# Kernel tuning notes

Hardware: AMD Instinct MI355X
Metric: run time of the kernel (lower is better)

The kernel has to match this reference:

```python
import jax, jax.numpy as jnp
import numpy as np

B, KEY, D, U, MODES = 16384, 64, 128, 128, 32

def setup_inputs() -> dict:
    key = jax.random.key(0)
    k1, k2, k3, k4, k5 = jax.random.split(key, 5)
    return {
        "key": jax.random.normal(k1, (B, KEY), dtype=jnp.float32),
        "x": jax.random.normal(k2, (B, D), dtype=jnp.float32),
        "sens": jnp.ones((MODES,), dtype=jnp.float32),
        "keys_map": jax.random.normal(k3, (MODES, KEY), dtype=jnp.float32),
        "kernels": jax.random.normal(k4, (MODES, D, U), dtype=jnp.float32) * 0.05,
        "biases": jax.random.normal(k5, (MODES, U), dtype=jnp.float32) * 0.05,
    }

def reference(key, x, sens, keys_map, kernels, biases):
    # key: [B, KEY]; keys_map: [MODES, KEY]
    # Euclidean distance of each key to each mode's stored key.
    dist = jnp.sqrt(jnp.sum((key[:, None, :] - keys_map[None, :, :]) ** 2, axis=-1))  # [B, MODES]
    sim = jax.nn.softmax(sens / (dist + 1.0), axis=-1)  # [B, MODES]
    modes = kernels.shape[0]
    # Original: kernel_b = mean_m(sim[b,m] * kernels[m]); out_b = x_b @ kernel_b.
    # Reordered as GEMM-per-mode + weighted combine (same math):
    out = jnp.einsum('bm,bd,mdu->bu', sim, x, kernels) / modes  # [B, U]
    out = out + (sim @ biases) / modes  # mean over modes of sim-weighted biases
    return out
```

## Files before the change

### kernel.cpp

```cpp
#include <hip/hip_runtime.h>

#define BATCH 16384
#define KEYD  64
#define DDIM  128
#define UDIM  128
#define MODES 32

typedef __attribute__((ext_vector_type(8))) short bf16x8;
typedef __attribute__((ext_vector_type(4))) float f32x4;

__device__ __forceinline__ unsigned short f2bf(float f) {
  unsigned u = __float_as_uint(f);
  unsigned r = (u + 0x7FFFu + ((u >> 16) & 1u)) >> 16;
  return (unsigned short)r;
}

__device__ __forceinline__ void gld_lds16(const void* g, void* l) {
  __builtin_amdgcn_global_load_lds(
      (const __attribute__((address_space(1))) unsigned int*)g,
      (__attribute__((address_space(3))) unsigned int*)l, 16, 0, 0);
}

__global__ __launch_bounds__(256) void prep_sim_x(
    const float* __restrict__ key, const float* __restrict__ x,
    const float* __restrict__ sens, const float* __restrict__ keys_map,
    float* __restrict__ sim, unsigned short* __restrict__ x16) {
  __shared__ float kmT[KEYD * MODES];
  int t = threadIdx.x;
  for (int i = t; i < MODES * KEYD; i += 256) {
    int m = i >> 6, k = i & 63;
    kmT[k * MODES + m] = keys_map[i];
  }
  __syncthreads();

  int lane = t & 63;
  int wave = t >> 6;
  int half = lane >> 5;
  int m = lane & 31;
  int row = blockIdx.x * 8 + wave * 2 + half;

  const float* krow = key + (long)row * KEYD;
  float d2 = 0.f;
  #pragma unroll
  for (int k = 0; k < KEYD; ++k) {
    float diff = krow[k] - kmT[k * MODES + m];
    d2 += diff * diff;
  }
  float logit = sens[m] / (sqrtf(d2) + 1.0f);
  float mx = logit;
  #pragma unroll
  for (int off = 16; off > 0; off >>= 1) mx = fmaxf(mx, __shfl_xor(mx, off, 64));
  float e = __expf(logit - mx);
  float s = e;
  #pragma unroll
  for (int off = 16; off > 0; off >>= 1) s += __shfl_xor(s, off, 64);
  sim[(long)row * MODES + m] = e / s;

  const float4 xv = *(const float4*)(x + (long)row * DDIM + m * 4);
  ushort4 o;
  o.x = f2bf(xv.x); o.y = f2bf(xv.y); o.z = f2bf(xv.z); o.w = f2bf(xv.w);
  *(ushort4*)(x16 + (long)row * DDIM + m * 4) = o;
}

__global__ __launch_bounds__(256) void prep_wb(
    const float* __restrict__ kernels, const float* __restrict__ biases,
    unsigned short* __restrict__ kb16, unsigned short* __restrict__ bb16) {
  int t = blockIdx.x * 256 + threadIdx.x;
  if (t < MODES * 16 * UDIM) {
    int u = t & 127, kb = (t >> 7) & 15, m = t >> 11;
    const float* src = kernels + (long)((m * 16 + kb) * 8) * UDIM + u;
    ushort4 lo, hi;
    lo.x = f2bf(src[0 * UDIM]); lo.y = f2bf(src[1 * UDIM]);
    lo.z = f2bf(src[2 * UDIM]); lo.w = f2bf(src[3 * UDIM]);
    hi.x = f2bf(src[4 * UDIM]); hi.y = f2bf(src[5 * UDIM]);
    hi.z = f2bf(src[6 * UDIM]); hi.w = f2bf(src[7 * UDIM]);
    *(ushort4*)(kb16 + (long)t * 8) = lo;
    *(ushort4*)(kb16 + (long)t * 8 + 4) = hi;
  } else if (t < MODES * 16 * UDIM + 4 * UDIM) {
    int tb = t - MODES * 16 * UDIM;
    int u = tb & 127, kb = tb >> 7;
    const float* src = biases + kb * 8 * UDIM + u;
    ushort4 lo, hi;
    lo.x = f2bf(src[0 * UDIM]); lo.y = f2bf(src[1 * UDIM]);
    lo.z = f2bf(src[2 * UDIM]); lo.w = f2bf(src[3 * UDIM]);
    hi.x = f2bf(src[4 * UDIM]); hi.y = f2bf(src[5 * UDIM]);
    hi.z = f2bf(src[6 * UDIM]); hi.w = f2bf(src[7 * UDIM]);
    *(ushort4*)(bb16 + (long)tb * 8) = lo;
    *(ushort4*)(bb16 + (long)tb * 8 + 4) = hi;
  }
}

__global__ __launch_bounds__(256, 2) void gemm_poly(
    const unsigned short* __restrict__ x16, const unsigned short* __restrict__ kb16,
    const unsigned short* __restrict__ bb16, const float* __restrict__ sim,
    float* __restrict__ out) {
  __shared__ alignas(16) unsigned short bsh[16 * UDIM * 8];
  __shared__ alignas(16) float simT[8][128];

  const int t = threadIdx.x;
  const int lane = t & 63, w = t >> 6;
  const int q = lane >> 4, l16 = lane & 15;
  const int wrow = (w >> 1) * 64, wcol = (w & 1) * 64;
  const long bm = (long)blockIdx.x * 128;
  const int split = blockIdx.y;

  {
    int rrow = t >> 1, mg = (t & 1) * 4;
    const float4 v = *(const float4*)(sim + (bm + rrow) * MODES + split * 8 + mg);
    simT[mg + 0][rrow] = v.x; simT[mg + 1][rrow] = v.y;
    simT[mg + 2][rrow] = v.z; simT[mg + 3][rrow] = v.w;
  }

  bf16x8 aF[4][4];
  #pragma unroll
  for (int rt = 0; rt < 4; ++rt)
    #pragma unroll
    for (int ks = 0; ks < 4; ++ks)
      aF[rt][ks] = *(const bf16x8*)(x16 + (bm + wrow + rt * 16 + l16) * DDIM + ks * 32 + q * 8);

  f32x4 acc[4][4] = {};

  for (int mi = 0; mi < 8; ++mi) {
    const int m = split * 8 + mi;
    __syncthreads();
    const unsigned short* src = kb16 + (long)m * (16 * UDIM * 8);
    #pragma unroll
    for (int i = 0; i < 8; ++i) {
      int off = (t + i * 256) * 8;
      gld_lds16(src + off, bsh + off);
    }
    __syncthreads();

    bf16x8 bF[4][4];
    #pragma unroll
    for (int ks = 0; ks < 4; ++ks)
      #pragma unroll
      for (int ct = 0; ct < 4; ++ct)
        bF[ks][ct] = *(const bf16x8*)&bsh[(((ks * 4 + q) * UDIM) + wcol + ct * 16 + l16) * 8];

    #pragma unroll
    for (int rt = 0; rt < 4; ++rt) {
      f32x4 tmp[4] = {};
      #pragma unroll
      for (int ks = 0; ks < 4; ++ks)
        #pragma unroll
        for (int ct = 0; ct < 4; ++ct)
          tmp[ct] = __builtin_amdgcn_mfma_f32_16x16x32_bf16(aF[rt][ks], bF[ks][ct], tmp[ct], 0, 0, 0);
      const f32x4 s = *(const f32x4*)&simT[mi][wrow + rt * 16 + q * 4];
      #pragma unroll
      for (int ct = 0; ct < 4; ++ct)
        acc[rt][ct] += s * tmp[ct];
    }
  }

  if (split == 0) {
    bf16x8 sF[4];
    #pragma unroll
    for (int rt = 0; rt < 4; ++rt) {
      const float* sp = sim + (bm + wrow + rt * 16 + l16) * MODES + q * 8;
      bf16x8 f;
      #pragma unroll
      for (int j = 0; j < 8; ++j) f[j] = (short)f2bf(sp[j]);
      sF[rt] = f;
    }
    #pragma unroll
    for (int ct = 0; ct < 4; ++ct) {
      bf16x8 bb = *(const bf16x8*)(bb16 + (long)(q * UDIM + wcol + ct * 16 + l16) * 8);
      #pragma unroll
      for (int rt = 0; rt < 4; ++rt)
        acc[rt][ct] = __builtin_amdgcn_mfma_f32_16x16x32_bf16(sF[rt], bb, acc[rt][ct], 0, 0, 0);
    }
  }

  #pragma unroll
  for (int rt = 0; rt < 4; ++rt)
    #pragma unroll
    for (int ct = 0; ct < 4; ++ct) {
      long row = bm + wrow + rt * 16 + q * 4;
      int col = wcol + ct * 16 + l16;
      #pragma unroll
      for (int r = 0; r < 4; ++r)
        atomicAdd(out + (row + r) * UDIM + col, acc[rt][ct][r] * (1.0f / MODES));
    }
}

extern "C" void kernel_launch(void* const* d_in, const int* in_sizes, int n_in,
                              void* d_out, int out_size, void* d_ws, size_t ws_size,
                              hipStream_t stream) {
  const float* key      = (const float*)d_in[0];
  const float* x        = (const float*)d_in[1];
  const float* sens     = (const float*)d_in[2];
  const float* keys_map = (const float*)d_in[3];
  const float* kernels  = (const float*)d_in[4];
  const float* biases   = (const float*)d_in[5];
  float* out = (float*)d_out;

  char* ws = (char*)d_ws;
  float*          sim  = (float*)ws;
  unsigned short* x16  = (unsigned short*)(ws + (2u << 20));
  unsigned short* kb16 = (unsigned short*)(ws + (6u << 20));
  unsigned short* bb16 = (unsigned short*)(ws + (7u << 20));

  hipMemsetAsync(out, 0, (size_t)BATCH * UDIM * sizeof(float), stream);
  prep_sim_x<<<BATCH / 8, 256, 0, stream>>>(key, x, sens, keys_map, sim, x16);
  prep_wb<<<(MODES * 16 * UDIM + 4 * UDIM + 255) / 256, 256, 0, stream>>>(kernels, biases, kb16, bb16);
  gemm_poly<<<dim3(BATCH / 128, 4), 256, 0, stream>>>(x16, kb16, bb16, sim, out);
}
```

Before: 130.9 us.

## Double-buffer per-mode weight tiles in LDS and stage key rows in shared memory

The GEMM kernel now keeps two LDS buffers for the per-mode bf16 weight tiles. It prefetches mode mi+1 with global_load_lds while computing on mode mi, which removes one barrier per iteration and hides load latency behind the MFMA work. The prep kernel now handles 16 rows per block and stages the key rows in shared memory, so the transposed keys_map load is amortized over twice as many rows and per-lane strided global key reads are avoided. The cost is doubled LDS use in the GEMM, which could limit occupancy. Overlap may also be reduced if the compiler inserts conservative waits on the async LDS loads.

Measured after the change: 129.0 us. Within noise of the previous version (-1.5%).

```diff
diff --git a/kernel.cpp b/kernel.cpp
--- a/kernel.cpp
+++ b/kernel.cpp
@@ -26,40 +26,48 @@
     const float* __restrict__ sens, const float* __restrict__ keys_map,
     float* __restrict__ sim, unsigned short* __restrict__ x16) {
   __shared__ float kmT[KEYD * MODES];
-  int t = threadIdx.x;
+  __shared__ float kr[16][KEYD];
+  const int t = threadIdx.x;
   for (int i = t; i < MODES * KEYD; i += 256) {
     int m = i >> 6, k = i & 63;
     kmT[k * MODES + m] = keys_map[i];
   }
+  {
+    const float4 v = *(const float4*)(key + (long)blockIdx.x * 16 * KEYD + t * 4);
+    *(float4*)(&kr[0][0] + t * 4) = v;
+  }
   __syncthreads();
 
-  int lane = t & 63;
-  int wave = t >> 6;
-  int half = lane >> 5;
-  int m = lane & 31;
-  int row = blockIdx.x * 8 + wave * 2 + half;
-
-  const float* krow = key + (long)row * KEYD;
-  float d2 = 0.f;
-  #pragma unroll
-  for (int k = 0; k < KEYD; ++k) {
-    float diff = krow[k] - kmT[k * MODES + m];
-    d2 += diff * diff;
-  }
-  float logit = sens[m] / (sqrtf(d2) + 1.0f);
-  float mx = logit;
-  #pragma unroll
-  for (int off = 16; off > 0; off >>= 1) mx = fmaxf(mx, __shfl_xor(mx, off, 64));
-  float e = __expf(logit - mx);
-  float s = e;
-  #pragma unroll
-  for (int off = 16; off > 0; off >>= 1) s += __shfl_xor(s, off, 64);
-  sim[(long)row * MODES + m] = e / s;
-
-  const float4 xv = *(const float4*)(x + (long)row * DDIM + m * 4);
-  ushort4 o;
-  o.x = f2bf(xv.x); o.y = f2bf(xv.y); o.z = f2bf(xv.z); o.w = f2bf(xv.w);
-  *(ushort4*)(x16 + (long)row * DDIM + m * 4) = o;
+  const int lane = t & 63, wave = t >> 6;
+  const int half = lane >> 5, m = lane & 31;
+  const float sv = sens[m];
+
+  #pragma unroll
+  for (int pass = 0; pass < 2; ++pass) {
+    const int rl = pass * 8 + wave * 2 + half;
+    const long row = (long)blockIdx.x * 16 + rl;
+
+    float d2 = 0.f;
+    #pragma unroll
+    for (int k = 0; k < KEYD; ++k) {
+      float diff = kr[rl][k] - kmT[k * MODES + m];
+      d2 += diff * diff;
+    }
+    float logit = sv / (sqrtf(d2) + 1.0f);
+    float mx = logit;
+    #pragma unroll
+    for (int off = 16; off > 0; off >>= 1) mx = fmaxf(mx, __shfl_xor(mx, off, 64));
+    float e = __expf(logit - mx);
+    float s = e;
+    #pragma unroll
+    for (int off = 16; off > 0; off >>= 1) s += __shfl_xor(s, off, 64);
+    sim[row * MODES + m] = e / s;
+
+    const float4 xv = *(const float4*)(x + row * DDIM + m * 4);
+    ushort4 o;
+    o.x = f2bf(xv.x); o.y = f2bf(xv.y); o.z = f2bf(xv.z); o.w = f2bf(xv.w);
+    *(ushort4*)(x16 + row * DDIM + m * 4) = o;
+  }
 }
 
 __global__ __launch_bounds__(256) void prep_wb(
@@ -94,7 +102,7 @@
     const unsigned short* __restrict__ x16, const unsigned short* __restrict__ kb16,
     const unsigned short* __restrict__ bb16, const float* __restrict__ sim,
     float* __restrict__ out) {
-  __shared__ alignas(16) unsigned short bsh[16 * UDIM * 8];
+  __shared__ alignas(16) unsigned short bsh[2][16 * UDIM * 8];
   __shared__ alignas(16) float simT[8][128];
 
   const int t = threadIdx.x;
@@ -118,25 +126,34 @@
     for (int ks = 0; ks < 4; ++ks)
       aF[rt][ks] = *(const bf16x8*)(x16 + (bm + wrow + rt * 16 + l16) * DDIM + ks * 32 + q * 8);
 
+  const unsigned short* kbase = kb16 + (long)(split * 8) * (16 * UDIM * 8);
+  #pragma unroll
+  for (int i = 0; i < 8; ++i) {
+    int off = (t + i * 256) * 8;
+    gld_lds16(kbase + off, &bsh[0][off]);
+  }
+
   f32x4 acc[4][4] = {};
 
   for (int mi = 0; mi < 8; ++mi) {
-    const int m = split * 8 + mi;
     __syncthreads();
-    const unsigned short* src = kb16 + (long)m * (16 * UDIM * 8);
-    #pragma unroll
-    for (int i = 0; i < 8; ++i) {
-      int off = (t + i * 256) * 8;
-      gld_lds16(src + off, bsh + off);
-    }
-    __syncthreads();
-
+    if (mi < 7) {
+      const unsigned short* src = kbase + (long)(mi + 1) * (16 * UDIM * 8);
+      unsigned short* dst = bsh[(mi + 1) & 1];
+      #pragma unroll
+      for (int i = 0; i < 8; ++i) {
+        int off = (t + i * 256) * 8;
+        gld_lds16(src + off, dst + off);
+      }
+    }
+
+    const unsigned short* bs = bsh[mi & 1];
     bf16x8 bF[4][4];
     #pragma unroll
     for (int ks = 0; ks < 4; ++ks)
       #pragma unroll
       for (int ct = 0; ct < 4; ++ct)
-        bF[ks][ct] = *(const bf16x8*)&bsh[(((ks * 4 + q) * UDIM) + wcol + ct * 16 + l16) * 8];
+        bF[ks][ct] = *(const bf16x8*)&bs[(((ks * 4 + q) * UDIM) + wcol + ct * 16 + l16) * 8];
 
     #pragma unroll
     for (int rt = 0; rt < 4; ++rt) {
@@ -202,7 +219,7 @@
   unsigned short* bb16 = (unsigned short*)(ws + (7u << 20));
 
   hipMemsetAsync(out, 0, (size_t)BATCH * UDIM * sizeof(float), stream);
-  prep_sim_x<<<BATCH / 8, 256, 0, stream>>>(key, x, sens, keys_map, sim, x16);
+  prep_sim_x<<<BATCH / 16, 256, 0, stream>>>(key, x, sens, keys_map, sim, x16);
   prep_wb<<<(MODES * 16 * UDIM + 4 * UDIM + 255) / 256, 256, 0, stream>>>(kernels, biases, kb16, bb16);
   gemm_poly<<<dim3(BATCH / 128, 4), 256, 0, stream>>>(x16, kb16, bb16, sim, out);
 }
```
